# Optimization experiments

Measured on AMD Instinct MI355X. Metric: run time of the kernel, lower is better.

Reference implementation:

```python
import jax, jax.numpy as jnp
import numpy as np
from jax import lax

NUM_HEADS = 8
KERNEL_SIZE = 7
PADDING_L = 3
EPS = 1e-12


def pow2_quantize(w):
    # LinearShift: weights constrained to sign * 2^round(log2|w|) (bit-shift arithmetic),
    # with straight-through estimator for gradients.
    wq = jnp.sign(w) * jnp.exp2(jnp.round(jnp.log2(jnp.abs(w) + EPS)))
    return w + lax.stop_gradient(wq - w)


def setup_inputs() -> dict:
    key = jax.random.key(0)
    k1, k2, k3 = jax.random.split(key, 3)
    T, B, C = 4096, 16, 512
    x = jax.random.normal(k1, (T, B, C), dtype=jnp.float32)
    shift_W = jax.random.normal(k2, (C, C), dtype=jnp.float32) * (1.0 / np.sqrt(C))
    shift_b = jnp.zeros((C,), dtype=jnp.float32)
    # xavier-uniform-ish init for the light-conv weight (H, K)
    lim = np.sqrt(6.0 / (NUM_HEADS + KERNEL_SIZE))
    weight = jax.random.uniform(k3, (NUM_HEADS, KERNEL_SIZE), minval=-lim, maxval=lim, dtype=jnp.float32)
    return {"x": x, "shift_W": shift_W, "shift_b": shift_b, "weight": weight}


def reference(x, shift_W, shift_b, weight):
    T, B, C = x.shape
    H, K = weight.shape
    R = C // H
    # 1) shift-linear: power-of-two quantized weights, y = x @ Wq^T + b  (T,B,C)
    Wq = pow2_quantize(shift_W)
    y = jnp.einsum("tbc,dc->tbd", x, Wq) + shift_b
    # 2) light (depthwise, head-shared) convolution along time
    xc = jnp.transpose(y, (1, 2, 0))  # (B, C, T)
    w = jax.nn.softmax(weight, axis=-1)  # weight_softmax=True
    # expand head kernels to per-channel depthwise kernels: (C, 1, K)
    w_full = jnp.repeat(w, R, axis=0)[:, None, :]
    out = lax.conv_general_dilated(
        xc, w_full,
        window_strides=(1,),
        padding=[(PADDING_L, K - 1 - PADDING_L)],
        dimension_numbers=("NCH", "OIH", "NCH"),
        feature_group_count=C,
    )  # (B, C, T)
    return jnp.transpose(out, (2, 0, 1))  # (T, B, C)
```

## Files before the change

### kernel.cpp

```cpp
#include <hip/hip_runtime.h>

constexpr int T_DIM = 4096;
constexpr int B_DIM = 16;
constexpr int C_DIM = 512;
constexpr int K_CONV = 7;
constexpr int M_DIM = T_DIM * B_DIM;
constexpr int BC = B_DIM * C_DIM;

typedef __attribute__((ext_vector_type(8))) short bf16x8;
typedef __attribute__((ext_vector_type(4))) float f32x4;
typedef __attribute__((ext_vector_type(8))) float f32x8;
typedef __attribute__((ext_vector_type(4))) unsigned int u32x4;
typedef __attribute__((ext_vector_type(2))) unsigned int u32x2;

__device__ __forceinline__ unsigned short f2bf(float f) {
  unsigned u = __float_as_uint(f);
  u += 0x7fffu + ((u >> 16) & 1u);
  return (unsigned short)(u >> 16);
}
__device__ __forceinline__ unsigned pack2(float a, float b) {
  return (unsigned)f2bf(a) | (((unsigned)f2bf(b)) << 16);
}

__global__ __launch_bounds__(256) void quantize_w(
    const float* __restrict__ W, unsigned short* __restrict__ Wq) {
  int i = blockIdx.x * 256 + threadIdx.x;
  float w = W[i];
  float a = fabsf(w) + 1e-12f;
  float q = exp2f(rintf(log2f(a)));
  q = (w > 0.f) ? q : ((w < 0.f) ? -q : 0.f);
  Wq[i] = f2bf(q);
}

constexpr int BK = 64;
constexpr int NSTEP = C_DIM / BK;

__global__ __launch_bounds__(256, 2) void gemm_bt(
    const float* __restrict__ X, const short* __restrict__ Bt,
    const float* __restrict__ bias, unsigned short* __restrict__ Y) {
  constexpr int K = C_DIM, N = C_DIM;
  __shared__ __align__(16) short As[2][128 * BK];
  __shared__ __align__(16) short Bs[2][128 * BK];

  const int id   = blockIdx.x;
  const int xcd  = id & 7;
  const int slot = id >> 3;
  const int nb   = slot & 3;
  const int mb   = xcd * 64 + (slot >> 2);
  const int m0 = mb * 128;
  const int n0 = nb * 128;

  const int t    = threadIdx.x;
  const int lane = t & 63;
  const int wid  = t >> 6;

  const int arow = t >> 4;
  const int acol = (t & 15) * 4;
  const float* pA = X + (long)(m0 + arow) * K + acol;
  const int awoff = ((((acol >> 3) ^ (arow & 7)) << 4) | ((acol & 4) << 1));

  const int brow = (wid << 5) + (lane >> 3);
  const int bcol = ((lane & 7) ^ ((lane >> 3) & 7)) * 8;
  const short* pB = Bt + (long)(n0 + brow) * K + bcol;

  const int fr = lane & 15;
  const int fq = lane >> 4;
  const int wm = (wid >> 1) * 64;
  const int wn = (wid & 1) * 64;
  const int sw0 = ((fq ^ (fr & 7)) << 4);
  const int sw1 = (((4 + fq) ^ (fr & 7)) << 4);

  f32x4 ax[8];
  f32x4 acc[4][4] = {};

  auto loadA = [&](int k0) {
#pragma unroll
    for (int j = 0; j < 8; ++j)
      ax[j] = *(const f32x4*)(pA + (long)j * 16 * K + k0);
  };
  auto stageB = [&](int bsel, int k0) {
#pragma unroll
    for (int i = 0; i < 4; ++i)
      __builtin_amdgcn_global_load_lds(
          (const __attribute__((address_space(1))) void*)(pB + (long)i * 8 * K + k0),
          (__attribute__((address_space(3))) void*)&Bs[bsel][wid * 2048 + i * 512],
          16, 0, 0);
  };
  auto writeA = [&](int bsel) {
    char* base = (char*)&As[bsel][0];
#pragma unroll
    for (int j = 0; j < 8; ++j) {
      u32x2 p;
      p[0] = pack2(ax[j][0], ax[j][1]);
      p[1] = pack2(ax[j][2], ax[j][3]);
      *(u32x2*)(base + (j * 16 + arow) * 128 + awoff) = p;
    }
  };
  auto compute = [&](int bsel) {
    const char* ab = (const char*)&As[bsel][0];
    const char* bb = (const char*)&Bs[bsel][0];
#pragma unroll
    for (int kk = 0; kk < 2; ++kk) {
      const int sw = kk ? sw1 : sw0;
      bf16x8 af[4], bfr[4];
#pragma unroll
      for (int i = 0; i < 4; ++i)
        af[i] = *(const bf16x8*)(ab + (wm + i * 16 + fr) * 128 + sw);
#pragma unroll
      for (int j = 0; j < 4; ++j)
        bfr[j] = *(const bf16x8*)(bb + (wn + j * 16 + fr) * 128 + sw);
#pragma unroll
      for (int i = 0; i < 4; ++i)
#pragma unroll
        for (int j = 0; j < 4; ++j)
          acc[i][j] = __builtin_amdgcn_mfma_f32_16x16x32_bf16(af[i], bfr[j], acc[i][j], 0, 0, 0);
    }
  };

  loadA(0);
  stageB(0, 0);
  writeA(0);
  __syncthreads();

#pragma unroll
  for (int s = 0; s < NSTEP; ++s) {
    const int buf = s & 1;
    if (s + 1 < NSTEP) {
      loadA((s + 1) * BK);
      stageB(buf ^ 1, (s + 1) * BK);
    }
    compute(buf);
    if (s + 1 < NSTEP) {
      writeA(buf ^ 1);
      __syncthreads();
    }
  }

#pragma unroll
  for (int j = 0; j < 4; ++j) {
    const int gn = n0 + wn + j * 16 + fr;
    const float bv = bias[gn];
#pragma unroll
    for (int i = 0; i < 4; ++i) {
#pragma unroll
      for (int r = 0; r < 4; ++r) {
        const int gm = m0 + wm + i * 16 + fq * 4 + r;
        Y[(long)gm * N + gn] = f2bf(acc[i][j][r] + bv);
      }
    }
  }
}

constexpr int CHT = 16;

__device__ __forceinline__ u32x4 loadY(const unsigned short* Y, int t, long off) {
  if ((unsigned)t < (unsigned)T_DIM)
    return *(const u32x4*)(Y + (long)t * BC + off);
  u32x4 z = {0u, 0u, 0u, 0u};
  return z;
}

__device__ __forceinline__ f32x8 unpack8(u32x4 u) {
  f32x8 r;
#pragma unroll
  for (int i = 0; i < 4; ++i) {
    unsigned w = u[i];
    r[2 * i]     = __uint_as_float(w << 16);
    r[2 * i + 1] = __uint_as_float(w & 0xffff0000u);
  }
  return r;
}

__global__ __launch_bounds__(256) void lconv(
    const unsigned short* __restrict__ Y, const float* __restrict__ W,
    float* __restrict__ O) {
  const int tid  = blockIdx.x * 256 + threadIdx.x;
  const int cvec = tid & 63;
  const int b    = (tid >> 6) & 15;
  const int tc   = tid >> 10;
  const int t0   = tc * CHT;
  const long off = (long)b * C_DIM + cvec * 8;
  const int h    = cvec >> 3;

  float wf[K_CONV];
  float mx = -1e30f;
#pragma unroll
  for (int k = 0; k < K_CONV; ++k) { wf[k] = W[h * K_CONV + k]; mx = fmaxf(mx, wf[k]); }
  float s = 0.f;
#pragma unroll
  for (int k = 0; k < K_CONV; ++k) { wf[k] = __expf(wf[k] - mx); s += wf[k]; }
  const float inv = 1.f / s;
#pragma unroll
  for (int k = 0; k < K_CONV; ++k) wf[k] *= inv;

  f32x8 win[K_CONV];
#pragma unroll
  for (int i = 0; i < 6; ++i) win[i] = unpack8(loadY(Y, t0 - 3 + i, off));

#pragma unroll
  for (int j = 0; j < CHT; ++j) {
    win[6] = unpack8(loadY(Y, t0 + 3 + j, off));
    f32x8 acc = win[0] * wf[0];
#pragma unroll
    for (int k = 1; k < K_CONV; ++k) acc += win[k] * wf[k];
    float* op = O + (long)(t0 + j) * BC + off;
    *(f32x4*)op       = f32x4{acc[0], acc[1], acc[2], acc[3]};
    *(f32x4*)(op + 4) = f32x4{acc[4], acc[5], acc[6], acc[7]};
#pragma unroll
    for (int k = 0; k < 6; ++k) win[k] = win[k + 1];
  }
}

extern "C" void kernel_launch(void* const* d_in, const int* in_sizes, int n_in,
                              void* d_out, int out_size, void* d_ws, size_t ws_size,
                              hipStream_t stream) {
  const float* x       = (const float*)d_in[0];
  const float* shift_W = (const float*)d_in[1];
  const float* shift_b = (const float*)d_in[2];
  const float* weight  = (const float*)d_in[3];
  float* out = (float*)d_out;

  unsigned short* Wq = (unsigned short*)d_ws;
  unsigned short* Y  = Wq + C_DIM * C_DIM;

  quantize_w<<<(C_DIM * C_DIM) / 256, 256, 0, stream>>>(shift_W, Wq);
  gemm_bt<<<(M_DIM / 128) * (C_DIM / 128), 256, 0, stream>>>(
      x, (const short*)Wq, shift_b, Y);
  lconv<<<(M_DIM / CHT) * (C_DIM / 8) / 256, 256, 0, stream>>>(Y, weight, out);
}
```

Before: 324.4 us.

## Halve GEMM K-tile for higher occupancy and restructure light conv per-timestep

The GEMM K-step drops from 64 to 32, with new swizzles and load mappings, and the kernel now requests 4 blocks per SM instead of 2, aiming for more latency hiding through occupancy. The light-conv kernel no longer slides a window over 16 timesteps per thread. Each thread now computes one timestep, loading all 7 taps directly, with block IDs remapped across XCDs and the softmax computed once per block into shared memory. The GEMM takes twice as many barrier steps, and the conv rereads each Y row about 7 times, leaning on the caches.

```diff
diff --git a/kernel.cpp b/kernel.cpp
--- a/kernel.cpp
+++ b/kernel.cpp
@@ -11,7 +11,6 @@
 typedef __attribute__((ext_vector_type(4))) float f32x4;
 typedef __attribute__((ext_vector_type(8))) float f32x8;
 typedef __attribute__((ext_vector_type(4))) unsigned int u32x4;
-typedef __attribute__((ext_vector_type(2))) unsigned int u32x2;
 
 __device__ __forceinline__ unsigned short f2bf(float f) {
   unsigned u = __float_as_uint(f);
@@ -32,10 +31,10 @@
   Wq[i] = f2bf(q);
 }
 
-constexpr int BK = 64;
+constexpr int BK = 32;
 constexpr int NSTEP = C_DIM / BK;
 
-__global__ __launch_bounds__(256, 2) void gemm_bt(
+__global__ __launch_bounds__(256, 4) void gemm_bt(
     const float* __restrict__ X, const short* __restrict__ Bt,
     const float* __restrict__ bias, unsigned short* __restrict__ Y) {
   constexpr int K = C_DIM, N = C_DIM;
@@ -54,67 +53,66 @@
   const int lane = t & 63;
   const int wid  = t >> 6;
 
-  const int arow = t >> 4;
-  const int acol = (t & 15) * 4;
-  const float* pA = X + (long)(m0 + arow) * K + acol;
-  const int awoff = ((((acol >> 3) ^ (arow & 7)) << 4) | ((acol & 4) << 1));
-
-  const int brow = (wid << 5) + (lane >> 3);
-  const int bcol = ((lane & 7) ^ ((lane >> 3) & 7)) * 8;
-  const short* pB = Bt + (long)(n0 + brow) * K + bcol;
+  const int ar = t >> 2;
+  const int ac = (t & 3) * 8;
+  const float* pA = X + (long)(m0 + ar) * K + ac;
+  const int awoff = (((t & 3) ^ ((ar >> 1) & 3)) << 4);
+
+  const int bc = ((t & 3) ^ ((t >> 3) & 3)) * 8;
+  const short* pB = Bt + (long)(n0 + (t >> 2)) * K + bc;
 
   const int fr = lane & 15;
   const int fq = lane >> 4;
   const int wm = (wid >> 1) * 64;
   const int wn = (wid & 1) * 64;
-  const int sw0 = ((fq ^ (fr & 7)) << 4);
-  const int sw1 = (((4 + fq) ^ (fr & 7)) << 4);
-
-  f32x4 ax[8];
+  const int sw = ((fq ^ ((fr >> 1) & 3)) << 4);
+
+  f32x4 ax[4];
   f32x4 acc[4][4] = {};
 
   auto loadA = [&](int k0) {
-#pragma unroll
-    for (int j = 0; j < 8; ++j)
-      ax[j] = *(const f32x4*)(pA + (long)j * 16 * K + k0);
+    ax[0] = *(const f32x4*)(pA + k0);
+    ax[1] = *(const f32x4*)(pA + k0 + 4);
+    ax[2] = *(const f32x4*)(pA + (long)64 * K + k0);
+    ax[3] = *(const f32x4*)(pA + (long)64 * K + k0 + 4);
   };
   auto stageB = [&](int bsel, int k0) {
 #pragma unroll
-    for (int i = 0; i < 4; ++i)
+    for (int i = 0; i < 2; ++i)
       __builtin_amdgcn_global_load_lds(
-          (const __attribute__((address_space(1))) void*)(pB + (long)i * 8 * K + k0),
-          (__attribute__((address_space(3))) void*)&Bs[bsel][wid * 2048 + i * 512],
+          (const __attribute__((address_space(1))) void*)(pB + (long)i * 64 * K + k0),
+          (__attribute__((address_space(3))) void*)&Bs[bsel][i * 2048 + wid * 512],
           16, 0, 0);
   };
   auto writeA = [&](int bsel) {
     char* base = (char*)&As[bsel][0];
-#pragma unroll
-    for (int j = 0; j < 8; ++j) {
-      u32x2 p;
-      p[0] = pack2(ax[j][0], ax[j][1]);
-      p[1] = pack2(ax[j][2], ax[j][3]);
-      *(u32x2*)(base + (j * 16 + arow) * 128 + awoff) = p;
-    }
+    u32x4 p0, p1;
+    p0[0] = pack2(ax[0][0], ax[0][1]);
+    p0[1] = pack2(ax[0][2], ax[0][3]);
+    p0[2] = pack2(ax[1][0], ax[1][1]);
+    p0[3] = pack2(ax[1][2], ax[1][3]);
+    p1[0] = pack2(ax[2][0], ax[2][1]);
+    p1[1] = pack2(ax[2][2], ax[2][3]);
+    p1[2] = pack2(ax[3][0], ax[3][1]);
+    p1[3] = pack2(ax[3][2], ax[3][3]);
+    *(u32x4*)(base + ar * 64 + awoff)        = p0;
+    *(u32x4*)(base + (64 + ar) * 64 + awoff) = p1;
   };
   auto compute = [&](int bsel) {
     const char* ab = (const char*)&As[bsel][0];
     const char* bb = (const char*)&Bs[bsel][0];
-#pragma unroll
-    for (int kk = 0; kk < 2; ++kk) {
-      const int sw = kk ? sw1 : sw0;
-      bf16x8 af[4], bfr[4];
-#pragma unroll
-      for (int i = 0; i < 4; ++i)
-        af[i] = *(const bf16x8*)(ab + (wm + i * 16 + fr) * 128 + sw);
+    bf16x8 af[4], bfr[4];
+#pragma unroll
+    for (int i = 0; i < 4; ++i)
+      af[i] = *(const bf16x8*)(ab + (wm + i * 16 + fr) * 64 + sw);
+#pragma unroll
+    for (int j = 0; j < 4; ++j)
+      bfr[j] = *(const bf16x8*)(bb + (wn + j * 16 + fr) * 64 + sw);
+#pragma unroll
+    for (int i = 0; i < 4; ++i)
 #pragma unroll
       for (int j = 0; j < 4; ++j)
-        bfr[j] = *(const bf16x8*)(bb + (wn + j * 16 + fr) * 128 + sw);
-#pragma unroll
-      for (int i = 0; i < 4; ++i)
-#pragma unroll
-        for (int j = 0; j < 4; ++j)
-          acc[i][j] = __builtin_amdgcn_mfma_f32_16x16x32_bf16(af[i], bfr[j], acc[i][j], 0, 0, 0);
-    }
+        acc[i][j] = __builtin_amdgcn_mfma_f32_16x16x32_bf16(af[i], bfr[j], acc[i][j], 0, 0, 0);
   };
 
   loadA(0);
@@ -151,8 +149,6 @@
   }
 }
 
-constexpr int CHT = 16;
-
 __device__ __forceinline__ u32x4 loadY(const unsigned short* Y, int t, long off) {
   if ((unsigned)t < (unsigned)T_DIM)
     return *(const u32x4*)(Y + (long)t * BC + off);
@@ -171,44 +167,50 @@
   return r;
 }
 
-__global__ __launch_bounds__(256) void lconv(
+__global__ __launch_bounds__(256, 4) void lconv(
     const unsigned short* __restrict__ Y, const float* __restrict__ W,
     float* __restrict__ O) {
-  const int tid  = blockIdx.x * 256 + threadIdx.x;
-  const int cvec = tid & 63;
-  const int b    = (tid >> 6) & 15;
-  const int tc   = tid >> 10;
-  const int t0   = tc * CHT;
+  __shared__ float sm_wf[8 * K_CONV];
+  if (threadIdx.x < 8) {
+    const int h = threadIdx.x;
+    float v[K_CONV];
+    float mx = -1e30f;
+#pragma unroll
+    for (int k = 0; k < K_CONV; ++k) { v[k] = W[h * K_CONV + k]; mx = fmaxf(mx, v[k]); }
+    float s = 0.f;
+#pragma unroll
+    for (int k = 0; k < K_CONV; ++k) { v[k] = __expf(v[k] - mx); s += v[k]; }
+    const float inv = 1.f / s;
+#pragma unroll
+    for (int k = 0; k < K_CONV; ++k) sm_wf[h * K_CONV + k] = v[k] * inv;
+  }
+
+  const int id   = blockIdx.x;
+  const int xcd  = id & 7;
+  const int slot = id >> 3;
+  const int b    = slot >> 7;
+  const int tl   = slot & 127;
+  const int t    = xcd * 512 + tl * 4 + (threadIdx.x >> 6);
+  const int cvec = threadIdx.x & 63;
   const long off = (long)b * C_DIM + cvec * 8;
   const int h    = cvec >> 3;
 
+  u32x4 v[K_CONV];
+#pragma unroll
+  for (int k = 0; k < K_CONV; ++k) v[k] = loadY(Y, t + k - 3, off);
+
+  __syncthreads();
   float wf[K_CONV];
-  float mx = -1e30f;
-#pragma unroll
-  for (int k = 0; k < K_CONV; ++k) { wf[k] = W[h * K_CONV + k]; mx = fmaxf(mx, wf[k]); }
-  float s = 0.f;
-#pragma unroll
-  for (int k = 0; k < K_CONV; ++k) { wf[k] = __expf(wf[k] - mx); s += wf[k]; }
-  const float inv = 1.f / s;
-#pragma unroll
-  for (int k = 0; k < K_CONV; ++k) wf[k] *= inv;
-
-  f32x8 win[K_CONV];
-#pragma unroll
-  for (int i = 0; i < 6; ++i) win[i] = unpack8(loadY(Y, t0 - 3 + i, off));
-
-#pragma unroll
-  for (int j = 0; j < CHT; ++j) {
-    win[6] = unpack8(loadY(Y, t0 + 3 + j, off));
-    f32x8 acc = win[0] * wf[0];
-#pragma unroll
-    for (int k = 1; k < K_CONV; ++k) acc += win[k] * wf[k];
-    float* op = O + (long)(t0 + j) * BC + off;
-    *(f32x4*)op       = f32x4{acc[0], acc[1], acc[2], acc[3]};
-    *(f32x4*)(op + 4) = f32x4{acc[4], acc[5], acc[6], acc[7]};
-#pragma unroll
-    for (int k = 0; k < 6; ++k) win[k] = win[k + 1];
-  }
+#pragma unroll
+  for (int k = 0; k < K_CONV; ++k) wf[k] = sm_wf[h * K_CONV + k];
+
+  f32x8 acc = unpack8(v[0]) * wf[0];
+#pragma unroll
+  for (int k = 1; k < K_CONV; ++k) acc += unpack8(v[k]) * wf[k];
+
+  float* op = O + (long)t * BC + off;
+  *(f32x4*)op       = f32x4{acc[0], acc[1], acc[2], acc[3]};
+  *(f32x4*)(op + 4) = f32x4{acc[4], acc[5], acc[6], acc[7]};
 }
 
 extern "C" void kernel_launch(void* const* d_in, const int* in_sizes, int n_in,
@@ -226,5 +228,5 @@
   quantize_w<<<(C_DIM * C_DIM) / 256, 256, 0, stream>>>(shift_W, Wq);
   gemm_bt<<<(M_DIM / 128) * (C_DIM / 128), 256, 0, stream>>>(
       x, (const short*)Wq, shift_b, Y);
-  lconv<<<(M_DIM / CHT) * (C_DIM / 8) / 256, 256, 0, stream>>>(Y, weight, out);
-}
+  lconv<<<M_DIM * (C_DIM / 8) / 256, 256, 0, stream>>>(Y, weight, out);
+}
```

Result: faster. 296.6 us (-8.6%).
